# Kernel tuning notes

Hardware: AMD Instinct MI355X
Metric: run time of the kernel (lower is better)

Reference implementation:

```python
import jax, jax.numpy as jnp
import numpy as np

INF = 1e10
EPS = 1e-5
B, S, H, NH = 4, 1024, 1024, 16


def _linear(x, W, b):
    return x @ W + b


def _layernorm(x, g, b):
    mean = x.mean(-1, keepdims=True)
    var = ((x - mean) ** 2).mean(-1, keepdims=True)  # biased, matches .pow(2).mean
    return g * (x - mean) / jnp.sqrt(var + EPS) + b


def _mha(xq, xkv, mask, Wq, bq, Wk, bk, Wv, bv, Wo, bo, num_head):
    Bq, Sq, Hd = xq.shape
    d = Hd // num_head
    scale = jnp.asarray(np.sqrt(d), xq.dtype)
    q = _linear(xq, Wq, bq).reshape(Bq, Sq, num_head, d).transpose(0, 2, 1, 3)
    k = _linear(xkv, Wk, bk).reshape(Bq, -1, num_head, d).transpose(0, 2, 1, 3)
    v = _linear(xkv, Wv, bv).reshape(Bq, -1, num_head, d).transpose(0, 2, 1, 3)
    scores = jnp.einsum('bhqd,bhkd->bhqk', q, k) / scale
    # mask [B,Skv] -> additive; NOTE: original divides (scores+mask) by scale AGAIN
    add = (1.0 - mask[:, None, None, :].astype(scores.dtype)) * (-INF)
    att = jax.nn.softmax((scores + add) / scale, axis=-1)
    out = jnp.einsum('bhqk,bhkd->bhqd', att, v).transpose(0, 2, 1, 3).reshape(Bq, Sq, Hd)
    return _linear(out, Wo, bo)


def _block(hidden_states, self_att_mask, cross_hidden_states, cross_att_mask,
           sWq, sbq, sWk, sbk, sWv, sbv, sWo, sbo,
           cWq, cbq, cWk, cbk, cWv, cbv, cWo, cbo,
           g, b, W1, b1, W2, b2, num_head):
    sa = _mha(hidden_states, hidden_states, self_att_mask,
              sWq, sbq, sWk, sbk, sWv, sbv, sWo, sbo, num_head)
    sa_n = _layernorm(sa + hidden_states, g, b)
    ca = _mha(sa_n, cross_hidden_states, cross_att_mask,
              cWq, cbq, cWk, cbk, cWv, cbv, cWo, cbo, num_head)
    # NOTE: residual uses the ORIGINAL hidden_states, matching the source
    h = _layernorm(ca + hidden_states, g, b)
    ff = _linear(jax.nn.relu(_linear(h, W1, b1)), W2, b2)
    return _layernorm(ff + h, g, b)


def setup_inputs() -> dict:
    key = jax.random.key(0)
    ks = jax.random.split(key, 20)
    std = 0.02
    def lin(k, din, dout):
        k1, k2 = jax.random.split(k)
        return (jax.random.normal(k1, (din, dout), jnp.float32) * std,
                jax.random.normal(k2, (dout,), jnp.float32) * std)
    inp = {
        'hidden_states': jax.random.normal(ks[0], (B, S, H), jnp.float32),
        'self_att_mask': jnp.ones((B, S), jnp.int32),
        'cross_hidden_states': jax.random.normal(ks[1], (B, S, H), jnp.float32),
        'cross_att_mask': jnp.ones((B, S), jnp.int32),
        'num_head': NH,
    }
    names = ['sWq sbq', 'sWk sbk', 'sWv sbv', 'sWo sbo',
             'cWq cbq', 'cWk cbk', 'cWv cbv', 'cWo cbo']
    for i, nm in enumerate(names):
        wn, bn = nm.split()
        W, bb = lin(ks[2 + i], H, H)
        inp[wn] = W
        inp[bn] = bb
    inp['g'] = jnp.ones((H,), jnp.float32)
    inp['b'] = jnp.zeros((H,), jnp.float32)
    inp['W1'], inp['b1'] = lin(ks[12], H, 4 * H)
    inp['W2'], inp['b2'] = lin(ks[13], 4 * H, H)
    return inp


def reference(hidden_states, self_att_mask, cross_hidden_states, cross_att_mask,
              num_head, sWq, sbq, sWk, sbk, sWv, sbv, sWo, sbo,
              cWq, cbq, cWk, cbk, cWv, cbv, cWo, cbo,
              g, b, W1, b1, W2, b2):
    return _block(hidden_states, self_att_mask, cross_hidden_states, cross_att_mask,
                  sWq, sbq, sWk, sbk, sWv, sbv, sWo, sbo,
                  cWq, cbq, cWk, cbk, cWv, cbv, cWo, cbo,
                  g, b, W1, b1, W2, b2, num_head)
```

## Files before the change

kernel.cpp:

```cpp
#include <hip/hip_runtime.h>
#include <hip/hip_bf16.h>


typedef float float4v __attribute__((ext_vector_type(4)));
typedef __bf16 bf16x8 __attribute__((ext_vector_type(8)));
typedef unsigned short ushort8 __attribute__((ext_vector_type(8)));
typedef unsigned int uint2v __attribute__((ext_vector_type(2)));

#define VBIG (1 << 29)

__device__ __forceinline__ unsigned short f2bf1(float f) {
    unsigned u = __builtin_bit_cast(unsigned, f);
    u += 0x7fffu + ((u >> 16) & 1u);
    return (unsigned short)(u >> 16);
}
__device__ __forceinline__ unsigned f2bf2(float lo, float hi) {
    unsigned a = __builtin_bit_cast(unsigned, lo);
    a += 0x7fffu + ((a >> 16) & 1u);
    unsigned b = __builtin_bit_cast(unsigned, hi);
    b += 0x7fffu + ((b >> 16) & 1u);
    return (a >> 16) | (b & 0xffff0000u);
}
__device__ __forceinline__ float4v bf4_to_f4(uint2v u) {
    float4v r;
    r.x = __builtin_bit_cast(float, (u.x & 0xffffu) << 16);
    r.y = __builtin_bit_cast(float, u.x & 0xffff0000u);
    r.z = __builtin_bit_cast(float, (u.y & 0xffffu) << 16);
    r.w = __builtin_bit_cast(float, u.y & 0xffff0000u);
    return r;
}
__device__ __forceinline__ bf16x8 ldsv8(const unsigned short* p) {
    return __builtin_bit_cast(bf16x8, *(const ushort8*)p);
}
__device__ __forceinline__ void async16(const unsigned short* g, unsigned short* l) {
    __builtin_amdgcn_global_load_lds(
        (const __attribute__((address_space(1))) unsigned int*)(g),
        (__attribute__((address_space(3))) unsigned int*)(l),
        16, 0, 0);
}

template <int RELU, int DBUF>
__device__ __forceinline__ void gemm_core(
    const unsigned short* __restrict__ A, const unsigned short* __restrict__ Bt,
    const float* __restrict__ bias, unsigned short* __restrict__ Cout,
    int m0, int n0, int K, int KL, int kbase, int ldc,
    float qs, int vrel, unsigned short* __restrict__ VTout, size_t outoff)
{
    __shared__ __align__(16) unsigned short As[(DBUF ? 2 : 1) * 128 * 64];
    __shared__ __align__(16) unsigned short Bs[(DBUF ? 2 : 1) * 128 * 64];

    const int tid = threadIdx.x;
    const int w = tid >> 6, lane = tid & 63;
    const int lr = lane & 15, quad = lane >> 4;
    const int wm = (w >> 1) * 64, wn = (w & 1) * 64;

    const int sr = lane >> 3, sc = lane & 7;
    const int fch = sc ^ sr;
    const unsigned short* Ag = A + (size_t)(m0 + w * 32 + sr) * K + kbase + fch * 8;
    const unsigned short* Bg = Bt + (size_t)(n0 + w * 32 + sr) * K + kbase + fch * 8;

    float4v acc[4][4];
#pragma unroll
    for (int i = 0; i < 4; i++)
#pragma unroll
        for (int j = 0; j < 4; j++) acc[i][j] = 0.f;

    const int ch0 = quad ^ (lr & 7);
    const int ch1 = (4 + quad) ^ (lr & 7);

    auto issue = [&](int buf, int k0) {
        unsigned short* Al = &As[buf * (128 * 64) + (w * 32) * 64];
        unsigned short* Bl = &Bs[buf * (128 * 64) + (w * 32) * 64];
#pragma unroll
        for (int i = 0; i < 4; i++) {
            async16(Ag + (size_t)(i * 8) * K + k0, Al + (i * 8) * 64);
            async16(Bg + (size_t)(i * 8) * K + k0, Bl + (i * 8) * 64);
        }
    };
    auto compute = [&](int buf) {
        const unsigned short* Ab = &As[buf * (128 * 64)];
        const unsigned short* Bb = &Bs[buf * (128 * 64)];
#pragma unroll
        for (int kk = 0; kk < 2; kk++) {
            const int ch = kk ? ch1 : ch0;
            bf16x8 af[4], bf[4];
#pragma unroll
            for (int i = 0; i < 4; i++) {
                af[i] = ldsv8(&Ab[(wm + i * 16 + lr) * 64 + ch * 8]);
                bf[i] = ldsv8(&Bb[(wn + i * 16 + lr) * 64 + ch * 8]);
            }
#pragma unroll
            for (int i = 0; i < 4; i++)
#pragma unroll
                for (int j = 0; j < 4; j++)
                    acc[i][j] = __builtin_amdgcn_mfma_f32_16x16x32_bf16(af[i], bf[j], acc[i][j], 0, 0, 0);
        }
    };

    if (DBUF) {
        const int NIT = KL >> 6;
        issue(0, 0);
        for (int it = 0; it < NIT; ++it) {
            const int nxt = it + 1;
            if (nxt < NIT) {
                issue(nxt & 1, nxt << 6);
                __builtin_amdgcn_sched_barrier(0);
                __builtin_amdgcn_s_waitcnt(0x0F78);
            } else {
                __builtin_amdgcn_sched_barrier(0);
                __builtin_amdgcn_s_waitcnt(0x0F70);
            }
            __builtin_amdgcn_s_barrier();
            __builtin_amdgcn_sched_barrier(0);
            compute(it & 1);
            __builtin_amdgcn_sched_barrier(0);
            __builtin_amdgcn_s_barrier();
            __builtin_amdgcn_sched_barrier(0);
        }
    } else {
        for (int k0 = 0; k0 < KL; k0 += 64) {
            issue(0, k0);
            __syncthreads();
            compute(0);
            __syncthreads();
        }
    }

    if (vrel >= 0) {
        const int crel = vrel + wn;
        const int hh = crel >> 6;
        const int bidx = (m0 + wm) >> 10;
        const int tbase = ((m0 + wm) & 1023) + quad * 16;
#pragma unroll
        for (int j = 0; j < 4; j++) {
            const float bv = bias ? bias[n0 + wn + j * 16 + lr] : 0.f;
            const int d = j * 16 + lr;
            unsigned short* vp = VTout + ((size_t)(bidx * 16 + hh) * 64 + d) * 1024 + tbase;
#pragma unroll
            for (int r = 0; r < 4; r++) {
                uint2v u = { f2bf2(acc[0][j][r] + bv, acc[1][j][r] + bv),
                             f2bf2(acc[2][j][r] + bv, acc[3][j][r] + bv) };
                *(uint2v*)(vp + r * 4) = u;
            }
        }
        return;
    }

#pragma unroll
    for (int j = 0; j < 4; j++) {
        const int col = n0 + wn + j * 16 + lr;
        const float bv = bias ? bias[col] : 0.f;
#pragma unroll
        for (int i = 0; i < 4; i++) {
            const int row0 = m0 + wm + i * 16 + quad * 4;
#pragma unroll
            for (int r = 0; r < 4; r++) {
                float v = (acc[i][j][r] + bv) * qs;
                if (RELU) v = fmaxf(v, 0.f);
                Cout[outoff + (size_t)(row0 + r) * ldc + col] = f2bf1(v);
            }
        }
    }
}

template <int RELU, int DBUF>
__global__ __launch_bounds__(256) void gemm_bt(
    const unsigned short* __restrict__ A, const unsigned short* __restrict__ Bt,
    const float* __restrict__ bias, unsigned short* __restrict__ Cout,
    int M, int N, int K, int ldc, int order, int qcols, int vcol0,
    unsigned short* __restrict__ VTout)
{
    const int m0 = (order ? blockIdx.x : blockIdx.y) * 128;
    const int n0 = (order ? blockIdx.y : blockIdx.x) * 128;
    const int KL = K / gridDim.z;
    const int kbase = blockIdx.z * KL;
    const float qs = (n0 < qcols) ? 0.015625f : 1.0f;
    const int vrel = (n0 >= vcol0) ? n0 - vcol0 : -1;
    const size_t outoff = (size_t)blockIdx.z * M * ldc;
    gemm_core<RELU, DBUF>(A, Bt, bias, Cout, m0, n0, K, KL, kbase, ldc,
                          qs, vrel, VTout, outoff);
}

__global__ __launch_bounds__(256) void gemm_cross(
    const unsigned short* __restrict__ SANb, const unsigned short* __restrict__ WtCWQ,
    const float* __restrict__ cbq, unsigned short* __restrict__ CQ,
    const unsigned short* __restrict__ cxb, const unsigned short* __restrict__ WtCKV,
    const float* __restrict__ biasC, unsigned short* __restrict__ CKb,
    unsigned short* __restrict__ VTc)
{
    const int m0 = blockIdx.x * 128;
    const int y = blockIdx.y;
    const unsigned short *Ax, *Btx;
    const float* bx;
    unsigned short* Cx = nullptr;
    unsigned short* vt = nullptr;
    int n0, ldc = 1024, vrel = -1;
    float qs = 1.0f;
    if (y < 8) {
        Ax = SANb; Btx = WtCWQ; bx = cbq; Cx = CQ; n0 = y * 128; qs = 0.015625f;
    } else {
        Ax = cxb; Btx = WtCKV; bx = biasC; n0 = (y - 8) * 128;
        if (n0 < 1024) Cx = CKb;
        else { vrel = n0 - 1024; vt = VTc; }
    }
    gemm_core<0, 0>(Ax, Btx, bx, Cx, m0, n0, 1024, 1024, 0, ldc, qs, vrel, vt, 0);
}

__global__ __launch_bounds__(256) void attn_mfma(
    const unsigned short* __restrict__ Q, int qs,
    const unsigned short* __restrict__ K, int kvs,
    const unsigned short* __restrict__ VT,
    const float* __restrict__ maskf,
    unsigned short* __restrict__ O)
{
    __shared__ __align__(16) unsigned short Ks[64 * 64];
    __shared__ __align__(16) unsigned short Vt[64 * 64];
    __shared__ __align__(16) unsigned short Pb[128 * 64];

    const int tid = threadIdx.x;
    const int b = blockIdx.z, h = blockIdx.y, q0 = blockIdx.x * 128;
    const int w = tid >> 6, lane = tid & 63;
    const int lr = lane & 15, quad = lane >> 4;
    const int wm = w * 32;
    const float4v zf = {0.f, 0.f, 0.f, 0.f};

    bf16x8 qf[2][2];
#pragma unroll
    for (int i = 0; i < 2; i++)
#pragma unroll
        for (int c = 0; c < 2; c++)
            qf[i][c] = ldsv8(Q + (size_t)(b * 1024 + q0 + wm + i * 16 + lr) * qs
                             + h * 64 + c * 32 + quad * 8);

    const int sr = lane >> 3, sc = lane & 7;
    const int fch = sc ^ sr;
    const int ch0 = quad ^ (lr & 7), ch1 = (4 + quad) ^ (lr & 7);
    const unsigned short* VTb = VT + (size_t)(b * 16 + h) * 64 * 1024;

    float4v oac[2][4];
    float lsum[2][4];
#pragma unroll
    for (int i = 0; i < 2; i++) {
#pragma unroll
        for (int j = 0; j < 4; j++) oac[i][j] = zf;
#pragma unroll
        for (int rr = 0; rr < 4; rr++) lsum[i][rr] = 0.f;
    }

    for (int kb = 0; kb < 16; ++kb) {
        const int s0 = kb * 64;
        __syncthreads();
#pragma unroll
        for (int i = 0; i < 2; i++) {
            async16(K + (size_t)(b * 1024 + s0 + w * 16 + i * 8 + sr) * kvs + h * 64 + fch * 8,
                    &Ks[(w * 16 + i * 8) * 64]);
            async16(VTb + (size_t)(w * 16 + i * 8 + sr) * 1024 + s0 + fch * 8,
                    &Vt[(w * 16 + i * 8) * 64]);
        }
        float mf[4];
#pragma unroll
        for (int j = 0; j < 4; j++)
            mf[j] = maskf[b * 1024 + s0 + j * 16 + lr];
        __syncthreads();

        float4v sa[2][4];
#pragma unroll
        for (int j = 0; j < 4; j++) {
            const int krow = j * 16 + lr;
            bf16x8 kf0 = ldsv8(&Ks[krow * 64 + ch0 * 8]);
            bf16x8 kf1 = ldsv8(&Ks[krow * 64 + ch1 * 8]);
            sa[0][j] = __builtin_amdgcn_mfma_f32_16x16x32_bf16(qf[0][0], kf0, zf, 0, 0, 0);
            sa[0][j] = __builtin_amdgcn_mfma_f32_16x16x32_bf16(qf[0][1], kf1, sa[0][j], 0, 0, 0);
            sa[1][j] = __builtin_amdgcn_mfma_f32_16x16x32_bf16(qf[1][0], kf0, zf, 0, 0, 0);
            sa[1][j] = __builtin_amdgcn_mfma_f32_16x16x32_bf16(qf[1][1], kf1, sa[1][j], 0, 0, 0);
        }

#pragma unroll
        for (int i = 0; i < 2; i++) {
#pragma unroll
            for (int rr = 0; rr < 4; rr++) {
                const float p0 = __expf(sa[i][0][rr]) * mf[0];
                const float p1 = __expf(sa[i][1][rr]) * mf[1];
                const float p2 = __expf(sa[i][2][rr]) * mf[2];
                const float p3 = __expf(sa[i][3][rr]) * mf[3];
                lsum[i][rr] += (p0 + p1) + (p2 + p3);
                const int row = wm + i * 16 + quad * 4 + rr;
                const int schp = (lr >> 1) ^ (row & 7);
                uint2v pk = { f2bf2(p0, p1), f2bf2(p2, p3) };
                *(uint2v*)&Pb[row * 64 + schp * 8 + (lr & 1) * 4] = pk;
            }
        }

        bf16x8 pf[2][2];
#pragma unroll
        for (int i = 0; i < 2; i++)
#pragma unroll
            for (int c = 0; c < 2; c++)
                pf[i][c] = ldsv8(&Pb[(wm + i * 16 + lr) * 64 + (c ? ch1 : ch0) * 8]);
#pragma unroll
        for (int j = 0; j < 4; j++) {
            bf16x8 vf0 = ldsv8(&Vt[(j * 16 + lr) * 64 + ch0 * 8]);
            bf16x8 vf1 = ldsv8(&Vt[(j * 16 + lr) * 64 + ch1 * 8]);
            oac[0][j] = __builtin_amdgcn_mfma_f32_16x16x32_bf16(pf[0][0], vf0, oac[0][j], 0, 0, 0);
            oac[0][j] = __builtin_amdgcn_mfma_f32_16x16x32_bf16(pf[0][1], vf1, oac[0][j], 0, 0, 0);
            oac[1][j] = __builtin_amdgcn_mfma_f32_16x16x32_bf16(pf[1][0], vf0, oac[1][j], 0, 0, 0);
            oac[1][j] = __builtin_amdgcn_mfma_f32_16x16x32_bf16(pf[1][1], vf1, oac[1][j], 0, 0, 0);
        }
    }

#pragma unroll
    for (int i = 0; i < 2; i++)
#pragma unroll
        for (int rr = 0; rr < 4; rr++) {
            float l = lsum[i][rr];
            l += __shfl_xor(l, 1);
            l += __shfl_xor(l, 2);
            l += __shfl_xor(l, 4);
            l += __shfl_xor(l, 8);
            const float inv = 1.0f / l;
            const int row = q0 + wm + i * 16 + quad * 4 + rr;
            unsigned short* op = O + (size_t)(b * 1024 + row) * 1024 + h * 64;
#pragma unroll
            for (int j = 0; j < 4; j++)
                op[j * 16 + lr] = f2bf1(oac[i][j][rr] * inv);
        }
}

#define PSTRIDE ((size_t)4096 * 1024)
__global__ __launch_bounds__(256) void add_ln_kernel(
    const unsigned short* __restrict__ P, int nparts, const float* __restrict__ lbias,
    const float* __restrict__ R,
    const float* __restrict__ g, const float* __restrict__ bb,
    float* __restrict__ outF, unsigned short* __restrict__ outB)
{
    const int row = blockIdx.x, tid = threadIdx.x;
    float4v z = ((const float4v*)(R + (size_t)row * 1024))[tid];
    for (int p = 0; p < nparts; ++p)
        z += bf4_to_f4(*(const uint2v*)(P + p * PSTRIDE + (size_t)row * 1024 + tid * 4));
    if (lbias) z += ((const float4v*)lbias)[tid];
    float s = z.x + z.y + z.z + z.w;
    float sq = z.x * z.x + z.y * z.y + z.z * z.z + z.w * z.w;
#pragma unroll
    for (int off = 32; off > 0; off >>= 1) {
        s += __shfl_down(s, off);
        sq += __shfl_down(sq, off);
    }
    __shared__ float ws[4], wsq[4];
    __shared__ float sm, sr;
    if ((tid & 63) == 0) { ws[tid >> 6] = s; wsq[tid >> 6] = sq; }
    __syncthreads();
    if (tid == 0) {
        float S1 = ws[0] + ws[1] + ws[2] + ws[3];
        float S2 = wsq[0] + wsq[1] + wsq[2] + wsq[3];
        float mean = S1 * (1.0f / 1024.0f);
        float var = S2 * (1.0f / 1024.0f) - mean * mean;
        sm = mean;
        sr = rsqrtf(var + 1e-5f);
    }
    __syncthreads();
    const float mean = sm, rstd = sr;
    const float4v* g4 = (const float4v*)g;
    const float4v* b4 = (const float4v*)bb;
    float4v res = g4[tid] * ((z - mean) * rstd) + b4[tid];
    if (outF) ((float4v*)(outF + (size_t)row * 1024))[tid] = res;
    if (outB) {
        uint2v u = { f2bf2(res.x, res.y), f2bf2(res.z, res.w) };
        *(uint2v*)(outB + (size_t)row * 1024 + tid * 4) = u;
    }
}

__device__ __forceinline__ void tconv_body(const float* __restrict__ S,
                                           unsigned short* __restrict__ D,
                                           int R, int C, int r0, int c0)
{
    __shared__ float tile[64][65];
    const int tid = threadIdx.x;
    const int tr = tid >> 4, tc4 = (tid & 15) * 4;
#pragma unroll
    for (int i = 0; i < 4; i++) {
        const int rr = i * 16 + tr;
        *(float4v*)&tile[rr][tc4] = *(const float4v*)(S + (size_t)(r0 + rr) * C + c0 + tc4);
    }
    __syncthreads();
#pragma unroll
    for (int i = 0; i < 4; i++) {
        const int dr = i * 16 + tr;
        float v0 = tile[tc4 + 0][dr];
        float v1 = tile[tc4 + 1][dr];
        float v2 = tile[tc4 + 2][dr];
        float v3 = tile[tc4 + 3][dr];
        uint2v u = { f2bf2(v0, v1), f2bf2(v2, v3) };
        *(uint2v*)(D + (size_t)(c0 + dr) * R + r0 + tc4) = u;
    }
}

__global__ __launch_bounds__(256) void prep_all(
    const float* __restrict__ x, const float* __restrict__ cx,
    unsigned short* __restrict__ xb, unsigned short* __restrict__ cxb,
    const float* s0, const float* s1, const float* s2, const float* s3,
    const float* s4, const float* s5, const float* s6, const float* s7,
    unsigned short* d0, unsigned short* d1, unsigned short* d2, unsigned short* d3,
    unsigned short* d4, unsigned short* d5, unsigned short* d6, unsigned short* d7,
    const float* __restrict__ W1, unsigned short* __restrict__ WtW1,
    const float* __restrict__ W2, unsigned short* __restrict__ WtW2,
    const float* __restrict__ sbq, const float* __restrict__ sbk, const float* __restrict__ sbv,
    const float* __restrict__ cbk, const float* __restrict__ cbv,
    const int* __restrict__ smask, const int* __restrict__ cmask,
    float* __restrict__ bq, float* __restrict__ bc,
    float* __restrict__ smf, float* __restrict__ cmf)
{
    const int bid = blockIdx.x, tid = threadIdx.x;
    if (bid < 8192) {
        const float* s = bid < 4096 ? x : cx;
        unsigned short* d = bid < 4096 ? xb : cxb;
        const size_t i = ((size_t)(bid & 4095) * 256 + tid) * 4;
        float4v v = *(const float4v*)(s + i);
        uint2v u = { f2bf2(v.x, v.y), f2bf2(v.z, v.w) };
        *(uint2v*)(d + i) = u;
    } else if (bid < 10240) {
        const int t = bid - 8192;
        const int which = t >> 8, sub = t & 255;
        const float* S;
        unsigned short* D;
        switch (which) {
            case 0: S = s0; D = d0; break;
            case 1: S = s1; D = d1; break;
            case 2: S = s2; D = d2; break;
            case 3: S = s3; D = d3; break;
            case 4: S = s4; D = d4; break;
            case 5: S = s5; D = d5; break;
            case 6: S = s6; D = d6; break;
            default: S = s7; D = d7; break;
        }
        tconv_body(S, D, 1024, 1024, (sub >> 4) * 64, (sub & 15) * 64);
    } else if (bid < 11264) {
        const int t = bid - 10240;
        tconv_body(W1, WtW1, 1024, 4096, (t >> 6) * 64, (t & 63) * 64);
    } else if (bid < 12288) {
        const int t = bid - 11264;
        tconv_body(W2, WtW2, 4096, 1024, (t & 63) * 64, (t >> 6) * 64);
    } else {
        const int i = (bid - 12288) * 256 + tid;
        if (i < 3072)
            bq[i] = i < 1024 ? sbq[i] : (i < 2048 ? sbk[i - 1024] : sbv[i - 2048]);
        else if (i < 5120) {
            const int j = i - 3072;
            bc[j] = j < 1024 ? cbk[j] : cbv[j - 1024];
        } else if (i < 9216)
            smf[i - 5120] = (float)smask[i - 5120];
        else
            cmf[i - 9216] = (float)cmask[i - 9216];
    }
}

extern "C" void kernel_launch(void* const* d_in, const int* in_sizes, int n_in,
                              void* d_out, int out_size, void* d_ws, size_t ws_size,
                              hipStream_t stream)
{
    const float* x     = (const float*)d_in[0];
    const int*   smask = (const int*)d_in[1];
    const float* cx    = (const float*)d_in[2];
    const int*   cmask = (const int*)d_in[3];
    const float* sWq = (const float*)d_in[5],  *sbq = (const float*)d_in[6];
    const float* sWk = (const float*)d_in[7],  *sbk = (const float*)d_in[8];
    const float* sWv = (const float*)d_in[9],  *sbv = (const float*)d_in[10];
    const float* sWo = (const float*)d_in[11], *sbo = (const float*)d_in[12];
    const float* cWq = (const float*)d_in[13], *cbq = (const float*)d_in[14];
    const float* cWk = (const float*)d_in[15], *cbk = (const float*)d_in[16];
    const float* cWv = (const float*)d_in[17], *cbv = (const float*)d_in[18];
    const float* cWo = (const float*)d_in[19], *cbo = (const float*)d_in[20];
    const float* g   = (const float*)d_in[21], *bb  = (const float*)d_in[22];
    const float* W1  = (const float*)d_in[23], *b1  = (const float*)d_in[24];
    const float* W2  = (const float*)d_in[25], *b2  = (const float*)d_in[26];
    float* out = (float*)d_out;

    const size_t MB = 1024 * 1024;
    unsigned char* ws = (unsigned char*)d_ws;
    unsigned short* xb   = (unsigned short*)(ws + 0 * MB);
    unsigned short* cxb  = (unsigned short*)(ws + 8 * MB);
    unsigned short* SANb = (unsigned short*)(ws + 16 * MB);
    unsigned short* CQ   = (unsigned short*)(ws + 24 * MB);
    unsigned short* MID  = (unsigned short*)(ws + 0 * MB);
    unsigned short* QK   = (unsigned short*)(ws + 32 * MB);
    unsigned short* VTs  = (unsigned short*)(ws + 48 * MB);
    unsigned short* P    = (unsigned short*)(ws + 32 * MB);
    unsigned short* CKb  = (unsigned short*)(ws + 56 * MB);
    unsigned short* VTc  = (unsigned short*)(ws + 64 * MB);
    unsigned short* T    = (unsigned short*)(ws + 72 * MB);
    float*          HH   = (float*)(ws + 80 * MB);
    unsigned short* HHb  = (unsigned short*)(ws + 96 * MB);
    unsigned short* WtQKV = (unsigned short*)(ws + 104 * MB);
    unsigned short* WtCKV = (unsigned short*)(ws + 110 * MB);
    unsigned short* WtSWO = (unsigned short*)(ws + 114 * MB);
    unsigned short* WtCWQ = (unsigned short*)(ws + 116 * MB);
    unsigned short* WtCWO = (unsigned short*)(ws + 118 * MB);
    unsigned short* WtW1  = (unsigned short*)(ws + 120 * MB);
    unsigned short* WtW2  = (unsigned short*)(ws + 128 * MB);
    float* biasQ = (float*)(ws + 136 * MB);
    float* biasC = (float*)(ws + 136 * MB + 16 * 1024);
    float* smf   = (float*)(ws + 136 * MB + 32 * 1024);
    float* cmf   = (float*)(ws + 136 * MB + 48 * 1024);

    dim3 blk(256);

    prep_all<<<12340, blk, 0, stream>>>(
        x, cx, xb, cxb,
        sWq, sWk, sWv, cWk, cWv, sWo, cWq, cWo,
        WtQKV, WtQKV + 1024 * 1024, WtQKV + 2 * 1024 * 1024,
        WtCKV, WtCKV + 1024 * 1024,
        WtSWO, WtCWQ, WtCWO,
        W1, WtW1, W2, WtW2,
        sbq, sbk, sbv, cbk, cbv, smask, cmask, biasQ, biasC, smf, cmf);

    gemm_bt<0, 0><<<dim3(32, 24), blk, 0, stream>>>(
        xb, WtQKV, biasQ, QK, 4096, 3072, 1024, 2048, 1, 1024, 2048, VTs);
    attn_mfma<<<dim3(8, 16, 4), blk, 0, stream>>>(QK, 2048, QK + 1024, 2048, VTs, smf, T);
    gemm_bt<0, 1><<<dim3(32, 8, 2), blk, 0, stream>>>(
        T, WtSWO, nullptr, P, 4096, 1024, 1024, 1024, 1, 0, VBIG, nullptr);
    add_ln_kernel<<<4096, blk, 0, stream>>>(P, 2, sbo, x, g, bb, nullptr, SANb);

    gemm_cross<<<dim3(32, 24), blk, 0, stream>>>(
        SANb, WtCWQ, cbq, CQ, cxb, WtCKV, biasC, CKb, VTc);
    attn_mfma<<<dim3(8, 16, 4), blk, 0, stream>>>(CQ, 1024, CKb, 1024, VTc, cmf, T);
    gemm_bt<0, 1><<<dim3(32, 8, 2), blk, 0, stream>>>(
        T, WtCWO, nullptr, P, 4096, 1024, 1024, 1024, 1, 0, VBIG, nullptr);
    add_ln_kernel<<<4096, blk, 0, stream>>>(P, 2, cbo, x, g, bb, HH, HHb);

    gemm_bt<1, 0><<<dim3(32, 32), blk, 0, stream>>>(
        HHb, WtW1, b1, MID, 4096, 4096, 1024, 4096, 0, 0, VBIG, nullptr);
    gemm_bt<0, 1><<<dim3(32, 8, 2), blk, 0, stream>>>(
        MID, WtW2, nullptr, P, 4096, 1024, 4096, 1024, 1, 0, VBIG, nullptr);
    add_ln_kernel<<<4096, blk, 0, stream>>>(P, 2, b2, HH, g, bb, out, nullptr);
}
```

Before: 474.0 us.

## Replace GEMMs with 256x256 8-wave pipelined kernel and 4-way split-K

```diff
diff --git a/kernel.cpp b/kernel.cpp
--- a/kernel.cpp
+++ b/kernel.cpp
@@ -39,109 +39,110 @@
         16, 0, 0);
 }
 
-template <int RELU, int DBUF>
-__device__ __forceinline__ void gemm_core(
+#define SCHED() __builtin_amdgcn_sched_barrier(0)
+#define SBAR() __builtin_amdgcn_s_barrier()
+#define WAIT_VM8() asm volatile("s_waitcnt vmcnt(8)" ::: "memory")
+#define WAIT_LGKM0() asm volatile("s_waitcnt lgkmcnt(0)" ::: "memory")
+
+#define PHASE(BUF, KK, MG, STCALL, W8) do {                                        \
+    bf16x8 af[4], bf[4];                                                           \
+    _Pragma("unroll")                                                              \
+    for (int m = 0; m < 4; m++)                                                    \
+        af[m] = ldsv8(&As[BUF][KK][(wm + MG * 64 + m * 16 + lr) * 32 + cho]);      \
+    _Pragma("unroll")                                                              \
+    for (int j = 0; j < 4; j++)                                                    \
+        bf[j] = ldsv8(&Bs[BUF][KK][(wn + j * 16 + lr) * 32 + cho]);                \
+    STCALL;                                                                        \
+    SCHED(); SBAR(); WAIT_LGKM0(); SCHED();                                        \
+    __builtin_amdgcn_s_setprio(1);                                                 \
+    _Pragma("unroll")                                                              \
+    for (int m = 0; m < 4; m++)                                                    \
+        _Pragma("unroll")                                                          \
+        for (int j = 0; j < 4; j++)                                                \
+            acc[MG * 4 + m][j] = __builtin_amdgcn_mfma_f32_16x16x32_bf16(          \
+                af[m], bf[j], acc[MG * 4 + m][j], 0, 0, 0);                        \
+    __builtin_amdgcn_s_setprio(0);                                                 \
+    SCHED();                                                                       \
+    if (W8) { WAIT_VM8(); }                                                        \
+    SCHED(); SBAR(); SCHED();                                                      \
+} while (0)
+
+template <int RELU>
+__device__ __forceinline__ void gemm8_core(
     const unsigned short* __restrict__ A, const unsigned short* __restrict__ Bt,
     const float* __restrict__ bias, unsigned short* __restrict__ Cout,
     int m0, int n0, int K, int KL, int kbase, int ldc,
     float qs, int vrel, unsigned short* __restrict__ VTout, size_t outoff)
 {
-    __shared__ __align__(16) unsigned short As[(DBUF ? 2 : 1) * 128 * 64];
-    __shared__ __align__(16) unsigned short Bs[(DBUF ? 2 : 1) * 128 * 64];
+    __shared__ __align__(16) unsigned short As[2][2][8192];
+    __shared__ __align__(16) unsigned short Bs[2][2][8192];
 
     const int tid = threadIdx.x;
     const int w = tid >> 6, lane = tid & 63;
     const int lr = lane & 15, quad = lane >> 4;
-    const int wm = (w >> 1) * 64, wn = (w & 1) * 64;
-
-    const int sr = lane >> 3, sc = lane & 7;
-    const int fch = sc ^ sr;
-    const unsigned short* Ag = A + (size_t)(m0 + w * 32 + sr) * K + kbase + fch * 8;
-    const unsigned short* Bg = Bt + (size_t)(n0 + w * 32 + sr) * K + kbase + fch * 8;
-
-    float4v acc[4][4];
-#pragma unroll
-    for (int i = 0; i < 4; i++)
-#pragma unroll
-        for (int j = 0; j < 4; j++) acc[i][j] = 0.f;
-
-    const int ch0 = quad ^ (lr & 7);
-    const int ch1 = (4 + quad) ^ (lr & 7);
-
-    auto issue = [&](int buf, int k0) {
-        unsigned short* Al = &As[buf * (128 * 64) + (w * 32) * 64];
-        unsigned short* Bl = &Bs[buf * (128 * 64) + (w * 32) * 64];
-#pragma unroll
-        for (int i = 0; i < 4; i++) {
-            async16(Ag + (size_t)(i * 8) * K + k0, Al + (i * 8) * 64);
-            async16(Bg + (size_t)(i * 8) * K + k0, Bl + (i * 8) * 64);
-        }
+    const int wm = (w >> 2) * 128, wn = (w & 3) * 64;
+    const int NT = KL >> 6;
+
+    const int srow = tid >> 2;
+    const int gco = ((tid & 3) ^ ((tid >> 3) & 3)) * 8;
+    const unsigned short* Ag = A + (size_t)(m0 + srow) * K + kbase + gco;
+    const unsigned short* Bg = Bt + (size_t)(n0 + srow) * K + kbase + gco;
+    const int ldst = w * 512;
+
+    float4v acc[8][4];
+#pragma unroll
+    for (int i = 0; i < 8; i++)
+#pragma unroll
+        for (int j = 0; j < 4; j++) acc[i][j] = (float4v){0.f, 0.f, 0.f, 0.f};
+
+    const int cho = (quad ^ ((lr >> 1) & 3)) * 8;
+
+    auto stA = [&](int t, int kh) {
+        unsigned short* l = &As[t & 1][kh][ldst];
+        const unsigned short* g = Ag + t * 64 + kh * 32;
+        async16(g, l);
+        async16(g + (size_t)128 * K, l + 4096);
     };
-    auto compute = [&](int buf) {
-        const unsigned short* Ab = &As[buf * (128 * 64)];
-        const unsigned short* Bb = &Bs[buf * (128 * 64)];
-#pragma unroll
-        for (int kk = 0; kk < 2; kk++) {
-            const int ch = kk ? ch1 : ch0;
-            bf16x8 af[4], bf[4];
-#pragma unroll
-            for (int i = 0; i < 4; i++) {
-                af[i] = ldsv8(&Ab[(wm + i * 16 + lr) * 64 + ch * 8]);
-                bf[i] = ldsv8(&Bb[(wn + i * 16 + lr) * 64 + ch * 8]);
-            }
-#pragma unroll
-            for (int i = 0; i < 4; i++)
-#pragma unroll
-                for (int j = 0; j < 4; j++)
-                    acc[i][j] = __builtin_amdgcn_mfma_f32_16x16x32_bf16(af[i], bf[j], acc[i][j], 0, 0, 0);
-        }
+    auto stB = [&](int t, int kh) {
+        unsigned short* l = &Bs[t & 1][kh][ldst];
+        const unsigned short* g = Bg + t * 64 + kh * 32;
+        async16(g, l);
+        async16(g + (size_t)128 * K, l + 4096);
     };
 
-    if (DBUF) {
-        const int NIT = KL >> 6;
-        issue(0, 0);
-        for (int it = 0; it < NIT; ++it) {
-            const int nxt = it + 1;
-            if (nxt < NIT) {
-                issue(nxt & 1, nxt << 6);
-                __builtin_amdgcn_sched_barrier(0);
-                __builtin_amdgcn_s_waitcnt(0x0F78);
-            } else {
-                __builtin_amdgcn_sched_barrier(0);
-                __builtin_amdgcn_s_waitcnt(0x0F70);
-            }
-            __builtin_amdgcn_s_barrier();
-            __builtin_amdgcn_sched_barrier(0);
-            compute(it & 1);
-            __builtin_amdgcn_sched_barrier(0);
-            __builtin_amdgcn_s_barrier();
-            __builtin_amdgcn_sched_barrier(0);
-        }
-    } else {
-        for (int k0 = 0; k0 < KL; k0 += 64) {
-            issue(0, k0);
-            __syncthreads();
-            compute(0);
-            __syncthreads();
-        }
+    stA(0, 0); stB(0, 0);
+    stA(0, 1); stB(0, 1);
+    stA(1, 0); stB(1, 0);
+    SCHED(); WAIT_VM8(); SCHED(); SBAR(); SCHED();
+
+    for (int u = 0; u < NT; ++u) {
+        const int buf = u & 1;
+        const int t1 = (u + 1 < NT) ? u + 1 : NT - 1;
+        const int t2 = (u + 2 < NT) ? u + 2 : NT - 1;
+        PHASE(buf, 0, 0, stA(t1, 1), 0);
+        PHASE(buf, 0, 1, stB(t1, 1), 1);
+        PHASE(buf, 1, 0, stA(t2, 0), 0);
+        PHASE(buf, 1, 1, stB(t2, 0), 1);
     }
 
     if (vrel >= 0) {
         const int crel = vrel + wn;
         const int hh = crel >> 6;
         const int bidx = (m0 + wm) >> 10;
-        const int tbase = ((m0 + wm) & 1023) + quad * 16;
+        const int tb = ((m0 + wm) & 1023) + quad * 16;
 #pragma unroll
         for (int j = 0; j < 4; j++) {
             const float bv = bias ? bias[n0 + wn + j * 16 + lr] : 0.f;
             const int d = j * 16 + lr;
-            unsigned short* vp = VTout + ((size_t)(bidx * 16 + hh) * 64 + d) * 1024 + tbase;
-#pragma unroll
-            for (int r = 0; r < 4; r++) {
-                uint2v u = { f2bf2(acc[0][j][r] + bv, acc[1][j][r] + bv),
-                             f2bf2(acc[2][j][r] + bv, acc[3][j][r] + bv) };
-                *(uint2v*)(vp + r * 4) = u;
-            }
+            unsigned short* vp = VTout + ((size_t)(bidx * 16 + hh) * 64 + d) * 1024 + tb;
+#pragma unroll
+            for (int gg = 0; gg < 2; gg++)
+#pragma unroll
+                for (int r = 0; r < 4; r++) {
+                    uint2v u2 = { f2bf2(acc[gg * 4 + 0][j][r] + bv, acc[gg * 4 + 1][j][r] + bv),
+                                  f2bf2(acc[gg * 4 + 2][j][r] + bv, acc[gg * 4 + 3][j][r] + bv) };
+                    *(uint2v*)(vp + gg * 64 + r * 4) = u2;
+                }
         }
         return;
     }
@@ -151,7 +152,7 @@
         const int col = n0 + wn + j * 16 + lr;
         const float bv = bias ? bias[col] : 0.f;
 #pragma unroll
-        for (int i = 0; i < 4; i++) {
+        for (int i = 0; i < 8; i++) {
             const int row0 = m0 + wm + i * 16 + quad * 4;
 #pragma unroll
             for (int r = 0; r < 4; r++) {
@@ -163,47 +164,47 @@
     }
 }
 
-template <int RELU, int DBUF>
-__global__ __launch_bounds__(256) void gemm_bt(
+template <int RELU>
+__global__ __launch_bounds__(512, 1) void gemm8_bt(
     const unsigned short* __restrict__ A, const unsigned short* __restrict__ Bt,
     const float* __restrict__ bias, unsigned short* __restrict__ Cout,
-    int M, int N, int K, int ldc, int order, int qcols, int vcol0,
+    int M, int K, int ldc, int qcols, int vcol0,
     unsigned short* __restrict__ VTout)
 {
-    const int m0 = (order ? blockIdx.x : blockIdx.y) * 128;
-    const int n0 = (order ? blockIdx.y : blockIdx.x) * 128;
+    const int n0 = blockIdx.x * 256;
+    const int m0 = blockIdx.y * 256;
     const int KL = K / gridDim.z;
     const int kbase = blockIdx.z * KL;
     const float qs = (n0 < qcols) ? 0.015625f : 1.0f;
     const int vrel = (n0 >= vcol0) ? n0 - vcol0 : -1;
     const size_t outoff = (size_t)blockIdx.z * M * ldc;
-    gemm_core<RELU, DBUF>(A, Bt, bias, Cout, m0, n0, K, KL, kbase, ldc,
-                          qs, vrel, VTout, outoff);
-}
-
-__global__ __launch_bounds__(256) void gemm_cross(
+    gemm8_core<RELU>(A, Bt, bias, Cout, m0, n0, K, KL, kbase, ldc,
+                     qs, vrel, VTout, outoff);
+}
+
+__global__ __launch_bounds__(512, 1) void gemm8_cross(
     const unsigned short* __restrict__ SANb, const unsigned short* __restrict__ WtCWQ,
     const float* __restrict__ cbq, unsigned short* __restrict__ CQ,
     const unsigned short* __restrict__ cxb, const unsigned short* __restrict__ WtCKV,
     const float* __restrict__ biasC, unsigned short* __restrict__ CKb,
     unsigned short* __restrict__ VTc)
 {
-    const int m0 = blockIdx.x * 128;
-    const int y = blockIdx.y;
+    const int m0 = blockIdx.y * 256;
+    const int y = blockIdx.x;
     const unsigned short *Ax, *Btx;
     const float* bx;
     unsigned short* Cx = nullptr;
     unsigned short* vt = nullptr;
-    int n0, ldc = 1024, vrel = -1;
+    int n0, vrel = -1;
     float qs = 1.0f;
-    if (y < 8) {
-        Ax = SANb; Btx = WtCWQ; bx = cbq; Cx = CQ; n0 = y * 128; qs = 0.015625f;
+    if (y < 4) {
+        Ax = SANb; Btx = WtCWQ; bx = cbq; Cx = CQ; n0 = y * 256; qs = 0.015625f;
     } else {
-        Ax = cxb; Btx = WtCKV; bx = biasC; n0 = (y - 8) * 128;
+        Ax = cxb; Btx = WtCKV; bx = biasC; n0 = (y - 4) * 256;
         if (n0 < 1024) Cx = CKb;
         else { vrel = n0 - 1024; vt = VTc; }
     }
-    gemm_core<0, 0>(Ax, Btx, bx, Cx, m0, n0, 1024, 1024, 0, ldc, qs, vrel, vt, 0);
+    gemm8_core<0>(Ax, Btx, bx, Cx, m0, n0, 1024, 1024, 0, 1024, qs, vrel, vt, 0);
 }
 
 __global__ __launch_bounds__(256) void attn_mfma(
@@ -502,6 +503,7 @@
     float* cmf   = (float*)(ws + 136 * MB + 48 * 1024);
 
     dim3 blk(256);
+    dim3 blk8(512);
 
     prep_all<<<12340, blk, 0, stream>>>(
         x, cx, xb, cxb,
@@ -512,23 +514,23 @@
         W1, WtW1, W2, WtW2,
         sbq, sbk, sbv, cbk, cbv, smask, cmask, biasQ, biasC, smf, cmf);
 
-    gemm_bt<0, 0><<<dim3(32, 24), blk, 0, stream>>>(
-        xb, WtQKV, biasQ, QK, 4096, 3072, 1024, 2048, 1, 1024, 2048, VTs);
+    gemm8_bt<0><<<dim3(12, 16), blk8, 0, stream>>>(
+        xb, WtQKV, biasQ, QK, 4096, 1024, 2048, 1024, 2048, VTs);
     attn_mfma<<<dim3(8, 16, 4), blk, 0, stream>>>(QK, 2048, QK + 1024, 2048, VTs, smf, T);
-    gemm_bt<0, 1><<<dim3(32, 8, 2), blk, 0, stream>>>(
-        T, WtSWO, nullptr, P, 4096, 1024, 1024, 1024, 1, 0, VBIG, nullptr);
-    add_ln_kernel<<<4096, blk, 0, stream>>>(P, 2, sbo, x, g, bb, nullptr, SANb);
-
-    gemm_cross<<<dim3(32, 24), blk, 0, stream>>>(
+    gemm8_bt<0><<<dim3(4, 16, 4), blk8, 0, stream>>>(
+        T, WtSWO, nullptr, P, 4096, 1024, 1024, 0, VBIG, nullptr);
+    add_ln_kernel<<<4096, blk, 0, stream>>>(P, 4, sbo, x, g, bb, nullptr, SANb);
+
+    gemm8_cross<<<dim3(12, 16), blk8, 0, stream>>>(
         SANb, WtCWQ, cbq, CQ, cxb, WtCKV, biasC, CKb, VTc);
     attn_mfma<<<dim3(8, 16, 4), blk, 0, stream>>>(CQ, 1024, CKb, 1024, VTc, cmf, T);
-    gemm_bt<0, 1><<<dim3(32, 8, 2), blk, 0, stream>>>(
-        T, WtCWO, nullptr, P, 4096, 1024, 1024, 1024, 1, 0, VBIG, nullptr);
-    add_ln_kernel<<<4096, blk, 0, stream>>>(P, 2, cbo, x, g, bb, HH, HHb);
-
-    gemm_bt<1, 0><<<dim3(32, 32), blk, 0, stream>>>(
-        HHb, WtW1, b1, MID, 4096, 4096, 1024, 4096, 0, 0, VBIG, nullptr);
-    gemm_bt<0, 1><<<dim3(32, 8, 2), blk, 0, stream>>>(
-        MID, WtW2, nullptr, P, 4096, 1024, 4096, 1024, 1, 0, VBIG, nullptr);
-    add_ln_kernel<<<4096, blk, 0, stream>>>(P, 2, b2, HH, g, bb, out, nullptr);
-}
+    gemm8_bt<0><<<dim3(4, 16, 4), blk8, 0, stream>>>(
+        T, WtCWO, nullptr, P, 4096, 1024, 1024, 0, VBIG, nullptr);
+    add_ln_kernel<<<4096, blk, 0, stream>>>(P, 4, cbo, x, g, bb, HH, HHb);
+
+    gemm8_bt<1><<<dim3(16, 16), blk8, 0, stream>>>(
+        HHb, WtW1, b1, MID, 4096, 1024, 4096, 0, VBIG, nullptr);
+    gemm8_bt<0><<<dim3(4, 16, 4), blk8, 0, stream>>>(
+        MID, WtW2, nullptr, P, 4096, 4096, 1024, 0, VBIG, nullptr);
+    add_ln_kernel<<<4096, blk, 0, stream>>>(P, 4, b2, HH, g, bb, out, nullptr);
+}
```

Result: slower. 521.0 us (+9.9%).

## Double-buffer K/V tiles in attention with async prefetch and remapped grid

Applied to the files above, without the earlier changes.

```diff
diff --git a/kernel.cpp b/kernel.cpp
--- a/kernel.cpp
+++ b/kernel.cpp
@@ -213,17 +213,22 @@
     const float* __restrict__ maskf,
     unsigned short* __restrict__ O)
 {
-    __shared__ __align__(16) unsigned short Ks[64 * 64];
-    __shared__ __align__(16) unsigned short Vt[64 * 64];
+    __shared__ __align__(16) unsigned short Ks[2][64 * 64];
+    __shared__ __align__(16) unsigned short Vt[2][64 * 64];
     __shared__ __align__(16) unsigned short Pb[128 * 64];
-
+    __shared__ float msk[1024];
+
+    const int bid = blockIdx.x;
+    const int jdx = (bid & 7) * 64 + (bid >> 3);
+    const int q0 = (jdx & 7) * 128, h = (jdx >> 3) & 15, b = jdx >> 7;
     const int tid = threadIdx.x;
-    const int b = blockIdx.z, h = blockIdx.y, q0 = blockIdx.x * 128;
     const int w = tid >> 6, lane = tid & 63;
     const int lr = lane & 15, quad = lane >> 4;
     const int wm = w * 32;
     const float4v zf = {0.f, 0.f, 0.f, 0.f};
 
+    ((float4v*)msk)[tid] = ((const float4v*)(maskf + b * 1024))[tid];
+
     bf16x8 qf[2][2];
 #pragma unroll
     for (int i = 0; i < 2; i++)
@@ -237,43 +242,62 @@
     const int ch0 = quad ^ (lr & 7), ch1 = (4 + quad) ^ (lr & 7);
     const unsigned short* VTb = VT + (size_t)(b * 16 + h) * 64 * 1024;
 
+    __syncthreads();
+
     float4v oac[2][4];
     float lsum[2][4];
 #pragma unroll
     for (int i = 0; i < 2; i++) {
 #pragma unroll
-        for (int j = 0; j < 4; j++) oac[i][j] = zf;
+        for (int jj = 0; jj < 4; jj++) oac[i][jj] = zf;
 #pragma unroll
         for (int rr = 0; rr < 4; rr++) lsum[i][rr] = 0.f;
     }
 
-    for (int kb = 0; kb < 16; ++kb) {
+    auto issue = [&](int kb, int buf) {
         const int s0 = kb * 64;
-        __syncthreads();
 #pragma unroll
         for (int i = 0; i < 2; i++) {
             async16(K + (size_t)(b * 1024 + s0 + w * 16 + i * 8 + sr) * kvs + h * 64 + fch * 8,
-                    &Ks[(w * 16 + i * 8) * 64]);
+                    &Ks[buf][(w * 16 + i * 8) * 64]);
             async16(VTb + (size_t)(w * 16 + i * 8 + sr) * 1024 + s0 + fch * 8,
-                    &Vt[(w * 16 + i * 8) * 64]);
-        }
+                    &Vt[buf][(w * 16 + i * 8) * 64]);
+        }
+    };
+
+    issue(0, 0);
+    for (int kb = 0; kb < 16; ++kb) {
+        const int cur = kb & 1;
+        const int nxt = kb + 1;
+        if (nxt < 16) {
+            issue(nxt, nxt & 1);
+            __builtin_amdgcn_sched_barrier(0);
+            __builtin_amdgcn_s_waitcnt(0x0F74);
+        } else {
+            __builtin_amdgcn_sched_barrier(0);
+            __builtin_amdgcn_s_waitcnt(0x0F70);
+        }
+        __builtin_amdgcn_s_barrier();
+        __builtin_amdgcn_sched_barrier(0);
+
         float mf[4];
 #pragma unroll
-        for (int j = 0; j < 4; j++)
-            mf[j] = maskf[b * 1024 + s0 + j * 16 + lr];
-        __syncthreads();
+        for (int jj = 0; jj < 4; jj++)
+            mf[jj] = msk[kb * 64 + jj * 16 + lr];
 
         float4v sa[2][4];
-#pragma unroll
-        for (int j = 0; j < 4; j++) {
-            const int krow = j * 16 + lr;
-            bf16x8 kf0 = ldsv8(&Ks[krow * 64 + ch0 * 8]);
-            bf16x8 kf1 = ldsv8(&Ks[krow * 64 + ch1 * 8]);
-            sa[0][j] = __builtin_amdgcn_mfma_f32_16x16x32_bf16(qf[0][0], kf0, zf, 0, 0, 0);
-            sa[0][j] = __builtin_amdgcn_mfma_f32_16x16x32_bf16(qf[0][1], kf1, sa[0][j], 0, 0, 0);
-            sa[1][j] = __builtin_amdgcn_mfma_f32_16x16x32_bf16(qf[1][0], kf0, zf, 0, 0, 0);
-            sa[1][j] = __builtin_amdgcn_mfma_f32_16x16x32_bf16(qf[1][1], kf1, sa[1][j], 0, 0, 0);
-        }
+        __builtin_amdgcn_s_setprio(1);
+#pragma unroll
+        for (int jj = 0; jj < 4; jj++) {
+            const int krow = jj * 16 + lr;
+            bf16x8 kf0 = ldsv8(&Ks[cur][krow * 64 + ch0 * 8]);
+            bf16x8 kf1 = ldsv8(&Ks[cur][krow * 64 + ch1 * 8]);
+            sa[0][jj] = __builtin_amdgcn_mfma_f32_16x16x32_bf16(qf[0][0], kf0, zf, 0, 0, 0);
+            sa[0][jj] = __builtin_amdgcn_mfma_f32_16x16x32_bf16(qf[0][1], kf1, sa[0][jj], 0, 0, 0);
+            sa[1][jj] = __builtin_amdgcn_mfma_f32_16x16x32_bf16(qf[1][0], kf0, zf, 0, 0, 0);
+            sa[1][jj] = __builtin_amdgcn_mfma_f32_16x16x32_bf16(qf[1][1], kf1, sa[1][jj], 0, 0, 0);
+        }
+        __builtin_amdgcn_s_setprio(0);
 
 #pragma unroll
         for (int i = 0; i < 2; i++) {
@@ -297,15 +321,21 @@
 #pragma unroll
             for (int c = 0; c < 2; c++)
                 pf[i][c] = ldsv8(&Pb[(wm + i * 16 + lr) * 64 + (c ? ch1 : ch0) * 8]);
-#pragma unroll
-        for (int j = 0; j < 4; j++) {
-            bf16x8 vf0 = ldsv8(&Vt[(j * 16 + lr) * 64 + ch0 * 8]);
-            bf16x8 vf1 = ldsv8(&Vt[(j * 16 + lr) * 64 + ch1 * 8]);
-            oac[0][j] = __builtin_amdgcn_mfma_f32_16x16x32_bf16(pf[0][0], vf0, oac[0][j], 0, 0, 0);
-            oac[0][j] = __builtin_amdgcn_mfma_f32_16x16x32_bf16(pf[0][1], vf1, oac[0][j], 0, 0, 0);
-            oac[1][j] = __builtin_amdgcn_mfma_f32_16x16x32_bf16(pf[1][0], vf0, oac[1][j], 0, 0, 0);
-            oac[1][j] = __builtin_amdgcn_mfma_f32_16x16x32_bf16(pf[1][1], vf1, oac[1][j], 0, 0, 0);
-        }
+        __builtin_amdgcn_s_setprio(1);
+#pragma unroll
+        for (int jj = 0; jj < 4; jj++) {
+            bf16x8 vf0 = ldsv8(&Vt[cur][(jj * 16 + lr) * 64 + ch0 * 8]);
+            bf16x8 vf1 = ldsv8(&Vt[cur][(jj * 16 + lr) * 64 + ch1 * 8]);
+            oac[0][jj] = __builtin_amdgcn_mfma_f32_16x16x32_bf16(pf[0][0], vf0, oac[0][jj], 0, 0, 0);
+            oac[0][jj] = __builtin_amdgcn_mfma_f32_16x16x32_bf16(pf[0][1], vf1, oac[0][jj], 0, 0, 0);
+            oac[1][jj] = __builtin_amdgcn_mfma_f32_16x16x32_bf16(pf[1][0], vf0, oac[1][jj], 0, 0, 0);
+            oac[1][jj] = __builtin_amdgcn_mfma_f32_16x16x32_bf16(pf[1][1], vf1, oac[1][jj], 0, 0, 0);
+        }
+        __builtin_amdgcn_s_setprio(0);
+
+        __builtin_amdgcn_sched_barrier(0);
+        __builtin_amdgcn_s_barrier();
+        __builtin_amdgcn_sched_barrier(0);
     }
 
 #pragma unroll
@@ -321,8 +351,8 @@
             const int row = q0 + wm + i * 16 + quad * 4 + rr;
             unsigned short* op = O + (size_t)(b * 1024 + row) * 1024 + h * 64;
 #pragma unroll
-            for (int j = 0; j < 4; j++)
-                op[j * 16 + lr] = f2bf1(oac[i][j][rr] * inv);
+            for (int jj = 0; jj < 4; jj++)
+                op[jj * 16 + lr] = f2bf1(oac[i][jj][rr] * inv);
         }
 }
 
@@ -514,14 +544,14 @@
 
     gemm_bt<0, 0><<<dim3(32, 24), blk, 0, stream>>>(
         xb, WtQKV, biasQ, QK, 4096, 3072, 1024, 2048, 1, 1024, 2048, VTs);
-    attn_mfma<<<dim3(8, 16, 4), blk, 0, stream>>>(QK, 2048, QK + 1024, 2048, VTs, smf, T);
+    attn_mfma<<<512, blk, 0, stream>>>(QK, 2048, QK + 1024, 2048, VTs, smf, T);
     gemm_bt<0, 1><<<dim3(32, 8, 2), blk, 0, stream>>>(
         T, WtSWO, nullptr, P, 4096, 1024, 1024, 1024, 1, 0, VBIG, nullptr);
     add_ln_kernel<<<4096, blk, 0, stream>>>(P, 2, sbo, x, g, bb, nullptr, SANb);
 
     gemm_cross<<<dim3(32, 24), blk, 0, stream>>>(
         SANb, WtCWQ, cbq, CQ, cxb, WtCKV, biasC, CKb, VTc);
-    attn_mfma<<<dim3(8, 16, 4), blk, 0, stream>>>(CQ, 1024, CKb, 1024, VTc, cmf, T);
+    attn_mfma<<<512, blk, 0, stream>>>(CQ, 1024, CKb, 1024, VTc, cmf, T);
     gemm_bt<0, 1><<<dim3(32, 8, 2), blk, 0, stream>>>(
         T, WtCWO, nullptr, P, 4096, 1024, 1024, 1024, 1, 0, VBIG, nullptr);
     add_ln_kernel<<<4096, blk, 0, stream>>>(P, 2, cbo, x, g, bb, HH, HHb);
```

Measured after the change: 476.6 us. About the same (+0.5%).
